# Optimization experiments

Measured on AMD Instinct MI355X. Metric: run time of the kernel, lower is better.

## Reference

```python
import jax, jax.numpy as jnp
import numpy as np

N_U, N_I, D, RANK, NNZ = 100000, 50000, 64, 64, 1000000
L, TEMP, LAMBDA_1, DROPOUT, BATCH_USER, EPS = 2, 0.2, 0.2, 0.1, 2048, 0.05
B = 2048


def _leaky(x):
    return jnp.where(x >= 0, x, 0.5 * x)


def _l2norm(x):
    n = jnp.sqrt(jnp.sum(x * x, axis=1, keepdims=True))
    return x / jnp.maximum(n, 1e-12)


def setup_inputs() -> dict:
    key = jax.random.key(0)
    ks = jax.random.split(key, 24)
    xav = 0.05
    inp = {
        'E_u_0': jax.random.normal(ks[0], (N_U, D), jnp.float32) * xav,
        'E_i_0': jax.random.normal(ks[1], (N_I, D), jnp.float32) * xav,
        'svd_u': jax.random.normal(ks[2], (N_U, RANK), jnp.float32) * xav,
        'svd_v': jax.random.normal(ks[3], (N_I, RANK), jnp.float32) * xav,
        's': jax.random.uniform(ks[4], (RANK,), jnp.float32),
        'ut': jax.random.normal(ks[5], (RANK, N_U), jnp.float32) * xav,
        'vt': jax.random.normal(ks[6], (RANK, N_I), jnp.float32) * xav,
        'W_u': jax.random.normal(ks[7], (L, D, D), jnp.float32) * xav,
        'W_i': jax.random.normal(ks[8], (L, D, D), jnp.float32) * xav,
        'adj_vals': jax.random.uniform(ks[9], (NNZ,), jnp.float32),
        'drop_rand': jax.random.uniform(ks[10], (L, 2, NNZ), jnp.float32),
        'noise_u1': jax.random.uniform(ks[11], (N_U, RANK), jnp.float32),
        'noise_v1': jax.random.uniform(ks[12], (N_I, RANK), jnp.float32),
        'noise_u2': jax.random.uniform(ks[13], (N_U, RANK), jnp.float32),
        'noise_v2': jax.random.uniform(ks[14], (N_I, RANK), jnp.float32),
        'u_mask_raw': jax.random.uniform(ks[15], (L, B), jnp.float32),
        'i_mask_raw': jax.random.uniform(ks[16], (L, B), jnp.float32),
        'adj_rows': jax.random.randint(ks[17], (NNZ,), 0, N_U, jnp.int32),
        'adj_cols': jax.random.randint(ks[18], (NNZ,), 0, N_I, jnp.int32),
        'uids': jax.random.randint(ks[19], (B,), 0, N_U, jnp.int32),
        'iids': jax.random.randint(ks[20], (B,), 0, N_I, jnp.int32),
        'pos': jax.random.randint(ks[21], (B,), 0, N_I, jnp.int32),
        'neg': jax.random.randint(ks[22], (B,), 0, N_I, jnp.int32),
    }
    return inp


def _forward(E_u_0, E_i_0, svd_u, svd_v, s, ut, vt, W_u, W_i, adj_vals,
             drop_rand, noise_u1, noise_v1, noise_u2, noise_v2,
             u_mask_raw, i_mask_raw, adj_rows, adj_cols, uids, iids, pos, neg):
    # --- SVD low-rank augmentation with sign-aligned uniform noise ---
    def perturb(svd, noise):
        return svd + jnp.sign(svd) * _l2norm(noise) * EPS

    svd_u_1, svd_v_1 = perturb(svd_u, noise_u1), perturb(svd_v, noise_v1)
    svd_u_2, svd_v_2 = perturb(svd_u, noise_u2), perturb(svd_v, noise_v2)
    u_mul_s_1 = svd_u_1 * s  # [n_u, r] @ diag(s)
    v_mul_s_1 = svd_v_1 * s
    u_mul_s_2 = svd_u_2 * s
    v_mul_s_2 = svd_v_2 * s

    def spmm_drop(vals_mask_rand, E, seg_ids, gather_ids, n_out):
        keep = (vals_mask_rand >= DROPOUT).astype(adj_vals.dtype)
        dv = adj_vals * keep / (1.0 - DROPOUT)  # sparse dropout w/ rescale
        msgs = dv[:, None] * E[gather_ids]       # [nnz, d]
        return jax.ops.segment_sum(msgs, seg_ids, num_segments=n_out)

    E_u_list, E_i_list = [E_u_0], [E_i_0]
    G_u_1, G_i_1, G_u_2, G_i_2 = [None], [None], [None], [None]
    for layer in range(1, L + 1):
        Eu_p, Ei_p = E_u_list[layer - 1], E_i_list[layer - 1]
        Z_u = _leaky(spmm_drop(drop_rand[layer - 1, 0], Ei_p, adj_rows, adj_cols, N_U))
        Z_i = _leaky(spmm_drop(drop_rand[layer - 1, 1], Eu_p, adj_cols, adj_rows, N_I))
        vt_ei = vt @ Ei_p   # [r, d]
        ut_eu = ut @ Eu_p   # [r, d]
        G_u_1.append(_leaky(u_mul_s_1 @ vt_ei))
        G_i_1.append(_leaky(v_mul_s_1 @ ut_eu))
        G_u_2.append(_leaky(u_mul_s_2 @ vt_ei))
        G_i_2.append(_leaky(v_mul_s_2 @ ut_eu))
        E_u_list.append(Z_u + Eu_p)
        E_i_list.append(Z_i + Ei_p)

    E_u = sum(E_u_list)
    E_i = sum(E_i_list)

    # --- contrastive InfoNCE between the two augmented views ---
    def cl_loss(g1, g2, ids, W, mask_raw):
        mask = (mask_raw > 0.5).astype(g1.dtype)
        h1 = _l2norm(g1[ids]) @ W
        h2 = _l2norm(g2[ids]) @ W
        pos_score = jnp.exp(jnp.sum(h1 * h2, axis=1) / TEMP)
        neg_score = jnp.sum(jnp.exp(h1 @ h2.T / TEMP), axis=1)
        return jnp.sum(-jnp.log(pos_score / (neg_score + 1e-8) + 1e-8) * mask)

    loss_s = jnp.asarray(0.0, E_u.dtype)
    for lyr in range(1, L + 1):
        loss_s = loss_s + cl_loss(G_u_1[lyr], G_u_2[lyr], uids, W_u[lyr - 1], u_mask_raw[lyr - 1])
        loss_s = loss_s + cl_loss(G_i_1[lyr], G_i_2[lyr], iids, W_i[lyr - 1], i_mask_raw[lyr - 1])

    # --- BPR-style hinge loss (vectorized over the batch loop) ---
    u_emb = E_u[uids]
    pos_sc = jnp.sum(u_emb * E_i[pos], axis=1)
    neg_sc = jnp.sum(u_emb * E_i[neg], axis=1)
    loss_r = jnp.sum(jax.nn.relu(1.0 - pos_sc + neg_sc)) / BATCH_USER

    loss = loss_r + LAMBDA_1 * loss_s
    return (loss, loss_r, loss_s)


def reference(E_u_0, E_i_0, svd_u, svd_v, s, ut, vt, W_u, W_i, adj_vals,
              drop_rand, noise_u1, noise_v1, noise_u2, noise_v2,
              u_mask_raw, i_mask_raw, adj_rows, adj_cols, uids, iids, pos, neg):
    return _forward(E_u_0, E_i_0, svd_u, svd_v, s, ut, vt, W_u, W_i, adj_vals,
                    drop_rand, noise_u1, noise_v1, noise_u2, noise_v2,
                    u_mask_raw, i_mask_raw, adj_rows, adj_cols, uids, iids, pos, neg)
```

## Files before the change

kernel.cpp:

```cpp
#include <hip/hip_runtime.h>
#include <cstddef>

#define N_U   100000
#define N_I   50000
#define DD    64
#define NNZ_  1000000
#define LL    2
#define TEMP_ 0.2f
#define LAM1  0.2f
#define DROP_ 0.1f
#define EPS_  0.05f
#define BB    2048
#define KCH   320
#define NCH_I ((N_I + KCH - 1) / KCH)
#define NCH_U ((N_U + KCH - 1) / KCH)
#define REGION_SZ 2097152

#define NBK   391
#define SH_U  8
#define SH_I  7
#define C1_CHUNK   3072
#define C1_THREADS 512
#define C1_EPT     6
#define BH_BLOCKS  256

__device__ __forceinline__ float leaky(float x) { return x >= 0.0f ? x : 0.5f * x; }

__device__ __forceinline__ float waveReduceSum(float v) {
#pragma unroll
  for (int m = 32; m >= 1; m >>= 1) v += __shfl_xor(v, m, 64);
  return v;
}

__device__ __forceinline__ int rlanei(int v, int l) {
  return __builtin_amdgcn_readlane(v, l);
}
__device__ __forceinline__ float rlanef(float v, int l) {
  return __int_as_float(__builtin_amdgcn_readlane(__float_as_int(v), l));
}

__device__ __forceinline__ void gload_lds16(const float* g, float* l) {
  __builtin_amdgcn_global_load_lds(
      (const __attribute__((address_space(1))) void*)g,
      (__attribute__((address_space(3))) void*)l, 16, 0, 0);
}

__global__ void bhist(const int* __restrict__ rows, const int* __restrict__ cols,
                      int* __restrict__ bh) {
  __shared__ int lh[2 * NBK];
  int t = threadIdx.x;
  for (int j = t; j < 2 * NBK; j += 256) lh[j] = 0;
  __syncthreads();
  for (int e = blockIdx.x * 256 + t; e < NNZ_; e += BH_BLOCKS * 256) {
    atomicAdd(&lh[rows[e] >> SH_U], 1);
    atomicAdd(&lh[NBK + (cols[e] >> SH_I)], 1);
  }
  __syncthreads();
  for (int j = t; j < 2 * NBK; j += 256) bh[blockIdx.x * (2 * NBK) + j] = lh[j];
}

__global__ void bscan(const int* __restrict__ bh,
                      int* __restrict__ bbase_u, int* __restrict__ bbase_i,
                      int* __restrict__ bcur_u, int* __restrict__ bcur_i) {
  __shared__ int tot[2 * NBK];
  __shared__ int sc[512];
  int t = threadIdx.x;
  for (int j = t; j < 2 * NBK; j += 256) {
    int s = 0;
    for (int k = 0; k < BH_BLOCKS; ++k) s += bh[k * (2 * NBK) + j];
    tot[j] = s;
  }
  __syncthreads();
  sc[t] = (t < NBK) ? tot[t] : 0;
  sc[t + 256] = (t + 256 < NBK) ? tot[t + 256] : 0;
  __syncthreads();
  for (int ofs = 1; ofs < 512; ofs <<= 1) {
    int a = (t >= ofs) ? sc[t - ofs] : 0;
    int b = (t + 256 >= ofs) ? sc[t + 256 - ofs] : 0;
    __syncthreads();
    sc[t] += a; sc[t + 256] += b;
    __syncthreads();
  }
  if (t == 0) bbase_u[0] = 0;
  for (int j = t; j < NBK; j += 256) bbase_u[j + 1] = sc[j];
  __syncthreads();
  sc[t] = (t < NBK) ? tot[NBK + t] : 0;
  sc[t + 256] = (t + 256 < NBK) ? tot[NBK + t + 256] : 0;
  __syncthreads();
  for (int ofs = 1; ofs < 512; ofs <<= 1) {
    int a = (t >= ofs) ? sc[t - ofs] : 0;
    int b = (t + 256 >= ofs) ? sc[t + 256 - ofs] : 0;
    __syncthreads();
    sc[t] += a; sc[t + 256] += b;
    __syncthreads();
  }
  if (t == 0) bbase_i[0] = 0;
  for (int j = t; j < NBK; j += 256) bbase_i[j + 1] = sc[j];
  for (int j = t; j < NBK; j += 256) { bcur_u[j] = 0; bcur_i[j] = 0; }
}

__global__ __launch_bounds__(C1_THREADS)
void csr_bin(const int* __restrict__ rws, const int* __restrict__ oth,
             const float* __restrict__ vals,
             const float* __restrict__ dA, const float* __restrict__ dB,
             const int* __restrict__ bbase,
             int* __restrict__ bcur,
             float4* __restrict__ stg, int shift) {
  __shared__ float4 st[C1_CHUNK];
  __shared__ int hist[NBK], lbase[NBK], cur2[NBK], slab[NBK], lboff[NBK];
  __shared__ int sc[512];
  int t = threadIdx.x;
  int e0 = blockIdx.x * C1_CHUNK;
  int n = min(C1_CHUNK, NNZ_ - e0);
  for (int b = t; b < NBK; b += C1_THREADS) { hist[b] = 0; cur2[b] = 0; }
  __syncthreads();
  int myr[C1_EPT], myo[C1_EPT];
  float mk1[C1_EPT], mk2[C1_EPT];
#pragma unroll
  for (int k = 0; k < C1_EPT; ++k) {
    int li = t + k * C1_THREADS;
    if (li < n) {
      int e = e0 + li;
      int r = rws[e];
      myr[k] = r;
      myo[k] = oth[e];
      float v = vals[e] * (1.0f / (1.0f - DROP_));
      mk1[k] = (dA[e] >= DROP_) ? v : 0.0f;
      mk2[k] = (dB[e] >= DROP_) ? v : 0.0f;
      atomicAdd(&hist[r >> shift], 1);
    } else {
      myr[k] = -1;
    }
  }
  __syncthreads();
  sc[t] = (t < NBK) ? hist[t] : 0;
  __syncthreads();
  for (int ofs = 1; ofs < 512; ofs <<= 1) {
    int x = (t >= ofs) ? sc[t - ofs] : 0;
    __syncthreads();
    sc[t] += x;
    __syncthreads();
  }
  if (t < NBK) {
    lbase[t] = (t == 0) ? 0 : sc[t - 1];
    lboff[t] = bbase[t];
    if (hist[t] > 0) slab[t] = atomicAdd(&bcur[t], hist[t]);
  }
  __syncthreads();
#pragma unroll
  for (int k = 0; k < C1_EPT; ++k) {
    if (myr[k] >= 0) {
      int b = myr[k] >> shift;
      int pos = lbase[b] + atomicAdd(&cur2[b], 1);
      st[pos] = make_float4(__int_as_float(myo[k]), mk1[k], mk2[k],
                            __int_as_float(myr[k]));
    }
  }
  __syncthreads();
  for (int s = t; s < n; s += C1_THREADS) {
    float4 rec = st[s];
    int r = __float_as_int(rec.w);
    int b = r >> shift;
    stg[(size_t)lboff[b] + slab[b] + (s - lbase[b])] = rec;
  }
}

__global__ void csr_final(const float4* __restrict__ stg, const int* __restrict__ bbase,
                          float2* __restrict__ pay1, float2* __restrict__ pay2,
                          int* __restrict__ off, int N, int shift) {
  __shared__ int h[256], incl[256], cur[256];
  int b = blockIdx.x;
  int t = threadIdx.x;
  int r0 = b << shift;
  int nrows = min(1 << shift, N - r0);
  int lo = bbase[b], hi = bbase[b + 1];
  h[t] = 0; cur[t] = 0;
  __syncthreads();
  for (int i = lo + t; i < hi; i += 256)
    atomicAdd(&h[__float_as_int(stg[i].w) - r0], 1);
  __syncthreads();
  incl[t] = h[t];
  __syncthreads();
  for (int ofs = 1; ofs < 256; ofs <<= 1) {
    int a = (t >= ofs) ? incl[t - ofs] : 0;
    __syncthreads();
    incl[t] += a;
    __syncthreads();
  }
  if (b == 0 && t == 0) off[0] = 0;
  if (t < nrows) off[r0 + t + 1] = lo + incl[t];
  for (int i = lo + t; i < hi; i += 256) {
    float4 rec = stg[i];
    int L = __float_as_int(rec.w) - r0;
    int pos = lo + (incl[L] - h[L]) + atomicAdd(&cur[L], 1);
    pay1[pos] = make_float2(rec.x, rec.y);
    pay2[pos] = make_float2(rec.x, rec.z);
  }
}

__global__ void spmm_all(const int* __restrict__ off_u, const float2* __restrict__ pu,
                         const int* __restrict__ off_i, const float2* __restrict__ pi,
                         const float* __restrict__ Eu0, const float* __restrict__ Ei0,
                         float* __restrict__ EU1, float* __restrict__ EI1) {
  int wid = threadIdx.x >> 6, lane = threadIdx.x & 63;
  int r = blockIdx.x * 4 + wid;
  const int* off; const float2* pay;
  const float* Esrc; const float* base; float* out;
  if (r < N_U) {
    off = off_u; pay = pu; Esrc = Ei0; base = Eu0; out = EU1;
  } else {
    r -= N_U;
    if (r >= N_I) return;
    off = off_i; pay = pi; Esrc = Eu0; base = Ei0; out = EI1;
  }
  int i0 = off[r], i1 = off[r + 1];
  float acc = 0.0f;
  for (int p = i0; p < i1; p += 64) {
    int cn = min(64, i1 - p);
    float dvl = 0.0f; int gl = 0;
    if (lane < cn) {
      float2 pl = pay[p + lane];
      gl = __float_as_int(pl.x);
      dvl = pl.y;
    }
    int j = 0;
    for (; j + 7 < cn; j += 8) {
      float d[8]; int g[8]; float e[8];
#pragma unroll
      for (int q = 0; q < 8; ++q) { d[q] = rlanef(dvl, j + q); g[q] = rlanei(gl, j + q); }
#pragma unroll
      for (int q = 0; q < 8; ++q) e[q] = Esrc[(size_t)g[q] * DD + lane];
#pragma unroll
      for (int q = 0; q < 8; ++q) acc += d[q] * e[q];
    }
    for (; j + 3 < cn; j += 4) {
      float d[4]; int g[4]; float e[4];
#pragma unroll
      for (int q = 0; q < 4; ++q) { d[q] = rlanef(dvl, j + q); g[q] = rlanei(gl, j + q); }
#pragma unroll
      for (int q = 0; q < 4; ++q) e[q] = Esrc[(size_t)g[q] * DD + lane];
#pragma unroll
      for (int q = 0; q < 4; ++q) acc += d[q] * e[q];
    }
    for (; j < cn; ++j)
      acc += rlanef(dvl, j) * Esrc[(size_t)rlanei(gl, j) * DD + lane];
  }
  size_t o = (size_t)r * DD + lane;
  out[o] = base[o] + leaky(acc);
}

__global__ void spmm_batch3(const int* __restrict__ uids, const int* __restrict__ pos,
                            const int* __restrict__ neg,
                            const int* __restrict__ off_u, const float2* __restrict__ pu2,
                            const int* __restrict__ off_i, const float2* __restrict__ pi2,
                            const float* __restrict__ EU1, const float* __restrict__ EI1,
                            float* __restrict__ bu, float* __restrict__ bpos,
                            float* __restrict__ bneg) {
  int z = blockIdx.y;
  const int* ids = (z == 0) ? uids : ((z == 1) ? pos : neg);
  const int* off = (z == 0) ? off_u : off_i;
  const float2* pay = (z == 0) ? pu2 : pi2;
  const float* Esrc = (z == 0) ? EI1 : EU1;
  const float* base = (z == 0) ? EU1 : EI1;
  float* out = (z == 0) ? bu : ((z == 1) ? bpos : bneg);
  int wid = threadIdx.x >> 6, lane = threadIdx.x & 63;
  int i = blockIdx.x * 4 + wid;
  int r = ids[i];
  int i0 = off[r], i1 = off[r + 1];
  float acc = 0.0f;
  for (int p = i0; p < i1; p += 64) {
    int cn = min(64, i1 - p);
    float dvl = 0.0f; int gl = 0;
    if (lane < cn) {
      float2 pl = pay[p + lane];
      gl = __float_as_int(pl.x);
      dvl = pl.y;
    }
    int j = 0;
    for (; j + 7 < cn; j += 8) {
      float d[8]; int g[8]; float e[8];
#pragma unroll
      for (int q = 0; q < 8; ++q) { d[q] = rlanef(dvl, j + q); g[q] = rlanei(gl, j + q); }
#pragma unroll
      for (int q = 0; q < 8; ++q) e[q] = Esrc[(size_t)g[q] * DD + lane];
#pragma unroll
      for (int q = 0; q < 8; ++q) acc += d[q] * e[q];
    }
    for (; j + 3 < cn; j += 4) {
      float d[4]; int g[4]; float e[4];
#pragma unroll
      for (int q = 0; q < 4; ++q) { d[q] = rlanef(dvl, j + q); g[q] = rlanei(gl, j + q); }
#pragma unroll
      for (int q = 0; q < 4; ++q) e[q] = Esrc[(size_t)g[q] * DD + lane];
#pragma unroll
      for (int q = 0; q < 4; ++q) acc += d[q] * e[q];
    }
    for (; j < cn; ++j)
      acc += rlanef(dvl, j) * Esrc[(size_t)rlanei(gl, j) * DD + lane];
  }
  out[(size_t)i * DD + lane] = base[(size_t)r * DD + lane] + leaky(acc);
}

__global__ void gemm_tiled(const float* __restrict__ A0, const float* __restrict__ B0,
                           const float* __restrict__ A1, const float* __restrict__ B1,
                           float* __restrict__ Cp) {
  __shared__ __align__(16) float sA[2][4096];
  __shared__ __align__(16) float sB[2][4096];
  int bx = blockIdx.x;
  const float* A; const float* B; int N; int k0;
  if (bx < NCH_I) { A = A0; B = B0; N = N_I; k0 = bx * KCH; }
  else            { A = A1; B = B1; N = N_U; k0 = (bx - NCH_I) * KCH; }
  int t = threadIdx.x;
  int w = t >> 6, l = t & 63;
  int rseg = l >> 4;
  int c4 = (l & 15) * 4;
  int ti = t >> 4, tj = t & 15;
  int ti4 = ti * 4, tj4 = tj * 4;

  int NT = min(KCH / 64, (N - k0 + 63) >> 6);

  float acc[4][4];
#pragma unroll
  for (int x = 0; x < 4; ++x)
#pragma unroll
    for (int y = 0; y < 4; ++y) acc[x][y] = 0.0f;

  auto stage = [&](int tt, int b) {
    int kb = k0 + tt * 64;
    if (kb + 64 <= N) {
#pragma unroll
      for (int q = 0; q < 4; ++q) {
        int s = w * 4 + q;
        const float* ga = A + (size_t)(s * 4 + rseg) * N + kb + c4;
        gload_lds16(ga, &sA[b][s * 256]);
        const float* gb = B + (size_t)(kb + s * 4 + rseg) * DD + c4;
        gload_lds16(gb, &sB[b][s * 256]);
      }
    } else {
#pragma unroll
      for (int q = 0; q < 16; ++q) {
        int lin = t + q * 256;
        int r = lin >> 6, c = lin & 63;
        sA[b][lin] = (kb + c < N) ? A[(size_t)r * N + kb + c] : 0.0f;
        sB[b][lin] = (kb + r < N) ? B[(size_t)(kb + r) * DD + c] : 0.0f;
      }
    }
  };

  stage(0, 0);
  __syncthreads();
  int cur = 0;
  for (int tt = 0; tt < NT; ++tt) {
    if (tt + 1 < NT) stage(tt + 1, cur ^ 1);
    const float* cA = sA[cur];
    const float* cB = sB[cur];
#pragma unroll 8
    for (int k = 0; k < 64; ++k) {
      float4 b4 = *(const float4*)&cB[k * 64 + tj4];
      float a0 = cA[(ti4 + 0) * 64 + k];
      float a1 = cA[(ti4 + 1) * 64 + k];
      float a2 = cA[(ti4 + 2) * 64 + k];
      float a3 = cA[(ti4 + 3) * 64 + k];
      acc[0][0] += a0 * b4.x; acc[0][1] += a0 * b4.y; acc[0][2] += a0 * b4.z; acc[0][3] += a0 * b4.w;
      acc[1][0] += a1 * b4.x; acc[1][1] += a1 * b4.y; acc[1][2] += a1 * b4.z; acc[1][3] += a1 * b4.w;
      acc[2][0] += a2 * b4.x; acc[2][1] += a2 * b4.y; acc[2][2] += a2 * b4.z; acc[2][3] += a2 * b4.w;
      acc[3][0] += a3 * b4.x; acc[3][1] += a3 * b4.y; acc[3][2] += a3 * b4.z; acc[3][3] += a3 * b4.w;
    }
    __syncthreads();
    cur ^= 1;
  }

  float* cp = Cp + (size_t)bx * 4096;
#pragma unroll
  for (int x = 0; x < 4; ++x)
#pragma unroll
    for (int y = 0; y < 4; ++y)
      cp[(ti4 + x) * DD + tj4 + y] = acc[x][y];
}

__global__ void gemm_reduce_s1(const float* __restrict__ Cp, float* __restrict__ Cp2) {
  int y = blockIdx.y, z = blockIdx.z;
  const float* base = Cp + (y ? (size_t)NCH_I * 4096 : 0);
  int cnt = y ? NCH_U : NCH_I;
  int chunk = (cnt + 3) >> 2;
  int b0 = z * chunk, b1 = min(b0 + chunk, cnt);
  int idx = blockIdx.x * 256 + threadIdx.x;
  float s = 0.0f;
  for (int b = b0; b < b1; ++b) s += base[(size_t)b * 4096 + idx];
  Cp2[((size_t)(y * 4 + z)) * 4096 + idx] = s;
}

__global__ void gemm_reduce_s2(const float* __restrict__ Cp2,
                               float* __restrict__ C0, float* __restrict__ C1) {
  int y = blockIdx.y;
  float* C = y ? C1 : C0;
  int idx = blockIdx.x * 256 + threadIdx.x;
  float s = 0.0f;
#pragma unroll
  for (int z = 0; z < 4; ++z) s += Cp2[((size_t)(y * 4 + z)) * 4096 + idx];
  C[idx] = s;
}

__global__ void h_kernel2(const float* __restrict__ svd,
                          const float* __restrict__ n1, const float* __restrict__ n2,
                          const float* __restrict__ sdiag,
                          const float* __restrict__ Mb,
                          const float* __restrict__ Wb,
                          const int*   __restrict__ ids,
                          float*       __restrict__ hout) {
  int layer = blockIdx.y;
  const float* M = Mb + layer * 4096;
  const float* W = Wb + layer * 4096;
  int wid  = threadIdx.x >> 6;
  int lane = threadIdx.x & 63;
  int i = blockIdx.x * 4 + wid;
  int id = ids[i];
  float sv = svd[(size_t)id * DD + lane];
  float sgn = (sv > 0.0f) ? 1.0f : ((sv < 0.0f) ? -1.0f : 0.0f);
  float sd = sdiag[lane];

  float z1 = n1[(size_t)id * DD + lane];
  float z2 = n2[(size_t)id * DD + lane];
  float d1 = fmaxf(sqrtf(waveReduceSum(z1 * z1)), 1e-12f);
  float d2 = fmaxf(sqrtf(waveReduceSum(z2 * z2)), 1e-12f);
  float g1 = (sv + sgn * (z1 / d1) * EPS_) * sd;
  float g2 = (sv + sgn * (z2 / d2) * EPS_) * sd;

  float a1 = 0.0f, a2 = 0.0f;
#pragma unroll
  for (int k = 0; k < 64; ++k) {
    float m = M[k * DD + lane];
    a1 += rlanef(g1, k) * m;
    a2 += rlanef(g2, k) * m;
  }
  a1 = leaky(a1); a2 = leaky(a2);
  float s1 = fmaxf(sqrtf(waveReduceSum(a1 * a1)), 1e-12f);
  float s2 = fmaxf(sqrtf(waveReduceSum(a2 * a2)), 1e-12f);
  float gn1 = a1 / s1, gn2 = a2 / s2;

  float h1 = 0.0f, h2 = 0.0f;
#pragma unroll
  for (int k = 0; k < 64; ++k) {
    float w = W[k * DD + lane];
    h1 += rlanef(gn1, k) * w;
    h2 += rlanef(gn2, k) * w;
  }
  size_t b0 = ((size_t)(layer * 2 + 0) * BB + i) * DD + lane;
  size_t b1 = ((size_t)(layer * 2 + 1) * BB + i) * DD + lane;
  hout[b0] = h1;
  hout[b1] = h2;
}

__global__ void score_tiles(const float* __restrict__ hu, const float* __restrict__ hv,
                            float* __restrict__ negpart) {
  __shared__ float s1[64][65];
  __shared__ float s2[64][65];
  int z = blockIdx.z;
  int layer = z >> 1, side = z & 1;
  const float* hb = side ? hv : hu;
  const float* h1 = hb + (size_t)(layer * 2 + 0) * BB * DD;
  const float* h2 = hb + (size_t)(layer * 2 + 1) * BB * DD;
  int i0 = blockIdx.x * 64, j0 = blockIdx.y * 64;
  int t = threadIdx.x;
#pragma unroll
  for (int k = 0; k < 16; ++k) {
    int lin = t + k * 256;
    int r = lin >> 6, c = lin & 63;
    s1[r][c] = h1[(size_t)(i0 + r) * DD + c];
    s2[r][c] = h2[(size_t)(j0 + r) * DD + c];
  }
  __syncthreads();
  int ti = t >> 4, tj = t & 15;
  float acc[4][4];
#pragma unroll
  for (int x = 0; x < 4; ++x)
#pragma unroll
    for (int y = 0; y < 4; ++y) acc[x][y] = 0.0f;
  for (int d = 0; d < 64; ++d) {
    float a[4], b[4];
#pragma unroll
    for (int k = 0; k < 4; ++k) { a[k] = s1[ti * 4 + k][d]; b[k] = s2[tj * 4 + k][d]; }
#pragma unroll
    for (int x = 0; x < 4; ++x)
#pragma unroll
      for (int y = 0; y < 4; ++y) acc[x][y] += a[x] * b[y];
  }
  float rsum[4];
#pragma unroll
  for (int x = 0; x < 4; ++x) {
    float s = 0.0f;
#pragma unroll
    for (int y = 0; y < 4; ++y) s += expf(acc[x][y] * (1.0f / TEMP_));
    rsum[x] = s;
  }
  __syncthreads();
#pragma unroll
  for (int x = 0; x < 4; ++x) s1[ti * 4 + x][tj] = rsum[x];
  __syncthreads();
  if (t < 64) {
    float s = 0.0f;
#pragma unroll
    for (int c = 0; c < 16; ++c) s += s1[t][c];
    negpart[((size_t)z * 32 + blockIdx.y) * BB + i0 + t] = s;
  }
}

__global__ void score_loss(const float* __restrict__ hu, const float* __restrict__ hv,
                           const float* __restrict__ negpart,
                           const float* __restrict__ u_mask, const float* __restrict__ i_mask,
                           float* __restrict__ loss_acc) {
  __shared__ float red[256];
  int z = blockIdx.y;
  int layer = z >> 1, side = z & 1;
  const float* hb = side ? hv : hu;
  const float* h1 = hb + (size_t)(layer * 2 + 0) * BB * DD;
  const float* h2 = hb + (size_t)(layer * 2 + 1) * BB * DD;
  const float* mask = (side ? i_mask : u_mask) + layer * BB;
  int i = blockIdx.x * 256 + threadIdx.x;
  const float4* a = (const float4*)(h1 + (size_t)i * DD);
  const float4* b = (const float4*)(h2 + (size_t)i * DD);
  float pos = 0.0f;
#pragma unroll
  for (int k = 0; k < 16; ++k) {
    float4 av = a[k], bv = b[k];
    pos += av.x * bv.x + av.y * bv.y + av.z * bv.z + av.w * bv.w;
  }
  float ng = 0.0f;
  for (int jt = 0; jt < 32; ++jt) ng += negpart[((size_t)z * 32 + jt) * BB + i];
  float ps = expf(pos * (1.0f / TEMP_));
  float m = (mask[i] > 0.5f) ? 1.0f : 0.0f;
  float li = -logf(ps / (ng + 1e-8f) + 1e-8f) * m;
  red[threadIdx.x] = li;
  __syncthreads();
  for (int ofs = 128; ofs >= 1; ofs >>= 1) {
    if (threadIdx.x < ofs) red[threadIdx.x] += red[threadIdx.x + ofs];
    __syncthreads();
  }
  if (threadIdx.x == 0) unsafeAtomicAdd(loss_acc, red[0]);
}

__global__ void bpr_kernel(const float* __restrict__ Eu0, const float* __restrict__ EU1,
                           const float* __restrict__ bu,
                           const float* __restrict__ Ei0, const float* __restrict__ EI1,
                           const float* __restrict__ bpos, const float* __restrict__ bneg,
                           const int* __restrict__ uids, const int* __restrict__ pos,
                           const int* __restrict__ neg,
                           float* __restrict__ acc_r) {
  __shared__ float red[256];
  int i = blockIdx.x * 256 + threadIdx.x;
  const float4* u0 = (const float4*)(Eu0 + (size_t)uids[i] * DD);
  const float4* u1 = (const float4*)(EU1 + (size_t)uids[i] * DD);
  const float4* u2 = (const float4*)(bu  + (size_t)i * DD);
  const float4* p0 = (const float4*)(Ei0 + (size_t)pos[i] * DD);
  const float4* p1 = (const float4*)(EI1 + (size_t)pos[i] * DD);
  const float4* p2 = (const float4*)(bpos + (size_t)i * DD);
  const float4* n0 = (const float4*)(Ei0 + (size_t)neg[i] * DD);
  const float4* n1 = (const float4*)(EI1 + (size_t)neg[i] * DD);
  const float4* n2 = (const float4*)(bneg + (size_t)i * DD);
  float ps = 0.0f, ns = 0.0f;
#pragma unroll
  for (int k = 0; k < 16; ++k) {
    float4 ua = u0[k], ub = u1[k], uc = u2[k];
    float4 pa = p0[k], pb = p1[k], pc = p2[k];
    float4 na = n0[k], nb = n1[k], nc = n2[k];
    float ux = ua.x + ub.x + uc.x, uy = ua.y + ub.y + uc.y,
          uz = ua.z + ub.z + uc.z, uw = ua.w + ub.w + uc.w;
    ps += ux * (pa.x + pb.x + pc.x) + uy * (pa.y + pb.y + pc.y)
        + uz * (pa.z + pb.z + pc.z) + uw * (pa.w + pb.w + pc.w);
    ns += ux * (na.x + nb.x + nc.x) + uy * (na.y + nb.y + nc.y)
        + uz * (na.z + nb.z + nc.z) + uw * (na.w + nb.w + nc.w);
  }
  red[threadIdx.x] = fmaxf(1.0f - ps + ns, 0.0f);
  __syncthreads();
  for (int ofs = 128; ofs >= 1; ofs >>= 1) {
    if (threadIdx.x < ofs) red[threadIdx.x] += red[threadIdx.x + ofs];
    __syncthreads();
  }
  if (threadIdx.x == 0) unsafeAtomicAdd(acc_r, red[0]);
}

__global__ void finalize_kernel(const float* __restrict__ acc, float* __restrict__ out) {
  float lr = acc[0] / (float)BB;
  float ls = acc[1];
  out[0] = lr + LAM1 * ls;
  out[1] = lr;
  out[2] = ls;
}

extern "C" void kernel_launch(void* const* d_in, const int* in_sizes, int n_in,
                              void* d_out, int out_size, void* d_ws, size_t ws_size,
                              hipStream_t stream) {
  const float* E_u_0   = (const float*)d_in[0];
  const float* E_i_0   = (const float*)d_in[1];
  const float* svd_u   = (const float*)d_in[2];
  const float* svd_v   = (const float*)d_in[3];
  const float* sdiag   = (const float*)d_in[4];
  const float* ut      = (const float*)d_in[5];
  const float* vt      = (const float*)d_in[6];
  const float* W_u     = (const float*)d_in[7];
  const float* W_i     = (const float*)d_in[8];
  const float* adjv    = (const float*)d_in[9];
  const float* dropr   = (const float*)d_in[10];
  const float* noise_u1= (const float*)d_in[11];
  const float* noise_v1= (const float*)d_in[12];
  const float* noise_u2= (const float*)d_in[13];
  const float* noise_v2= (const float*)d_in[14];
  const float* u_mask  = (const float*)d_in[15];
  const float* i_mask  = (const float*)d_in[16];
  const int*   rows    = (const int*)d_in[17];
  const int*   cols    = (const int*)d_in[18];
  const int*   uids    = (const int*)d_in[19];
  const int*   iids    = (const int*)d_in[20];
  const int*   pos     = (const int*)d_in[21];
  const int*   neg     = (const int*)d_in[22];
  float* out = (float*)d_out;

  float* ws     = (float*)d_ws;
  float* EU1    = ws;
  float* EI1    = EU1 + (size_t)N_U * DD;
  float* vtei   = EI1 + (size_t)N_I * DD;
  float* uteu   = vtei + 2 * DD * DD;
  float* accs   = uteu + 2 * DD * DD;
  float* region = accs + 16;
  float* Cp   = region;
  float* Cp2  = Cp + (size_t)(NCH_I + NCH_U) * 4096;
  float* bu   = region;
  float* bpos = bu   + (size_t)BB * DD;
  float* bneg = bpos + (size_t)BB * DD;
  float* hu   = bneg + (size_t)BB * DD;
  float* hv   = hu   + (size_t)4 * BB * DD;
  float* negp = hv   + (size_t)4 * BB * DD;
  float2* pay1_u = (float2*)(region + (size_t)REGION_SZ);
  float2* pay2_u = pay1_u + NNZ_;
  float2* pay1_i = pay2_u + NNZ_;
  float2* pay2_i = pay1_i + NNZ_;
  int* off_u   = (int*)(pay2_i + NNZ_);
  int* off_i   = off_u + (N_U + 1);
  int* bcur_u  = off_i + (N_I + 1);
  int* bcur_i  = bcur_u + NBK;
  int* bbase_u = bcur_i + NBK;
  int* bbase_i = bbase_u + (NBK + 1);
  float4* stg_u = (float4*)ws;
  float4* stg_i = stg_u + NNZ_;
  int* bh = (int*)region;

  const int TB = 256;
  dim3 blk(TB);
  int row_grid = BB / 4;

  hipMemsetAsync(accs, 0, 16 * sizeof(float), stream);

  bhist<<<BH_BLOCKS, blk, 0, stream>>>(rows, cols, bh);
  bscan<<<1, blk, 0, stream>>>(bh, bbase_u, bbase_i, bcur_u, bcur_i);
  {
    int c1g = (NNZ_ + C1_CHUNK - 1) / C1_CHUNK;
    csr_bin<<<c1g, C1_THREADS, 0, stream>>>(rows, cols, adjv,
        dropr, dropr + (size_t)2 * NNZ_, bbase_u, bcur_u, stg_u, SH_U);
    csr_bin<<<c1g, C1_THREADS, 0, stream>>>(cols, rows, adjv,
        dropr + (size_t)NNZ_, dropr + (size_t)3 * NNZ_, bbase_i, bcur_i, stg_i, SH_I);
    csr_final<<<NBK, blk, 0, stream>>>(stg_u, bbase_u, pay1_u, pay2_u, off_u, N_U, SH_U);
    csr_final<<<NBK, blk, 0, stream>>>(stg_i, bbase_i, pay1_i, pay2_i, off_i, N_I, SH_I);
  }

  gemm_tiled<<<NCH_I + NCH_U, blk, 0, stream>>>(vt, E_i_0, ut, E_u_0, Cp);
  gemm_reduce_s1<<<dim3(16, 2, 4), blk, 0, stream>>>(Cp, Cp2);
  gemm_reduce_s2<<<dim3(16, 2), blk, 0, stream>>>(Cp2, vtei, uteu);

  spmm_all<<<(N_U + N_I + 3) / 4, blk, 0, stream>>>(off_u, pay1_u, off_i, pay1_i,
                                                    E_u_0, E_i_0, EU1, EI1);

  gemm_tiled<<<NCH_I + NCH_U, blk, 0, stream>>>(vt, EI1, ut, EU1, Cp);
  gemm_reduce_s1<<<dim3(16, 2, 4), blk, 0, stream>>>(Cp, Cp2);
  gemm_reduce_s2<<<dim3(16, 2), blk, 0, stream>>>(Cp2, vtei + 4096, uteu + 4096);

  spmm_batch3<<<dim3(row_grid, 3), blk, 0, stream>>>(uids, pos, neg,
      off_u, pay2_u, off_i, pay2_i, EU1, EI1, bu, bpos, bneg);

  h_kernel2<<<dim3(row_grid, LL), blk, 0, stream>>>(svd_u, noise_u1, noise_u2, sdiag,
                                                    vtei, W_u, uids, hu);
  h_kernel2<<<dim3(row_grid, LL), blk, 0, stream>>>(svd_v, noise_v1, noise_v2, sdiag,
                                                    uteu, W_i, iids, hv);
  score_tiles<<<dim3(32, 32, 4), blk, 0, stream>>>(hu, hv, negp);
  score_loss<<<dim3(8, 4), blk, 0, stream>>>(hu, hv, negp, u_mask, i_mask, accs + 1);

  bpr_kernel<<<8, blk, 0, stream>>>(E_u_0, EU1, bu, E_i_0, EI1, bpos, bneg,
                                    uids, pos, neg, accs);

  finalize_kernel<<<1, 1, 0, stream>>>(accs, out);
}
```

Measured before the change: 624.7 us.

## Merge paired launches, vectorize SpMM gathers, parallelize BPR per wavefront

The user-side and item-side launches of csr_bin, csr_final and h_kernel2 are merged into single launches that pick the side from a grid dimension, which cuts launch overhead and lets both sides run at once. The SpMM gather now has each group of 16 lanes load a float4 slice of an embedding row, so one wavefront fetches four neighbours per step, and it sums the groups with xor shuffles. The BPR kernel moves from one thread per sample with serial float4 loops to one wavefront per sample with a wave reduction, giving more parallelism on a small batch. The new gather loop steps by 8 without tail handling and relies on lanes past the count carrying zero weights, which adds wasted loads on short rows.

```diff
diff --git a/kernel.cpp b/kernel.cpp
--- a/kernel.cpp
+++ b/kernel.cpp
@@ -100,12 +100,21 @@
 }
 
 __global__ __launch_bounds__(C1_THREADS)
-void csr_bin(const int* __restrict__ rws, const int* __restrict__ oth,
-             const float* __restrict__ vals,
-             const float* __restrict__ dA, const float* __restrict__ dB,
-             const int* __restrict__ bbase,
-             int* __restrict__ bcur,
-             float4* __restrict__ stg, int shift) {
+void csr_bin(const int* __restrict__ rows, const int* __restrict__ cols,
+             const float* __restrict__ vals, const float* __restrict__ dropr,
+             const int* __restrict__ bbase_u, const int* __restrict__ bbase_i,
+             int* __restrict__ bcur_u, int* __restrict__ bcur_i,
+             float4* __restrict__ stg_u, float4* __restrict__ stg_i) {
+  int side = blockIdx.y;
+  const int* rws = side ? cols : rows;
+  const int* oth = side ? rows : cols;
+  const float* dA = dropr + (side ? (size_t)NNZ_ : 0);
+  const float* dB = dropr + (side ? (size_t)3 * NNZ_ : (size_t)2 * NNZ_);
+  const int* bbase = side ? bbase_i : bbase_u;
+  int* bcur = side ? bcur_i : bcur_u;
+  float4* stg = side ? stg_i : stg_u;
+  int shift = side ? SH_I : SH_U;
+
   __shared__ float4 st[C1_CHUNK];
   __shared__ int hist[NBK], lbase[NBK], cur2[NBK], slab[NBK], lboff[NBK];
   __shared__ int sc[512];
@@ -165,9 +174,20 @@
   }
 }
 
-__global__ void csr_final(const float4* __restrict__ stg, const int* __restrict__ bbase,
-                          float2* __restrict__ pay1, float2* __restrict__ pay2,
-                          int* __restrict__ off, int N, int shift) {
+__global__ void csr_final(const float4* __restrict__ stg_u, const float4* __restrict__ stg_i,
+                          const int* __restrict__ bbase_u, const int* __restrict__ bbase_i,
+                          float2* __restrict__ pay1_u, float2* __restrict__ pay2_u,
+                          float2* __restrict__ pay1_i, float2* __restrict__ pay2_i,
+                          int* __restrict__ off_u, int* __restrict__ off_i) {
+  int side = blockIdx.y;
+  const float4* stg = side ? stg_i : stg_u;
+  const int* bbase = side ? bbase_i : bbase_u;
+  float2* pay1 = side ? pay1_i : pay1_u;
+  float2* pay2 = side ? pay2_i : pay2_u;
+  int* off = side ? off_i : off_u;
+  int N = side ? N_I : N_U;
+  int shift = side ? SH_I : SH_U;
+
   __shared__ int h[256], incl[256], cur[256];
   int b = blockIdx.x;
   int t = threadIdx.x;
@@ -198,23 +218,12 @@
   }
 }
 
-__global__ void spmm_all(const int* __restrict__ off_u, const float2* __restrict__ pu,
-                         const int* __restrict__ off_i, const float2* __restrict__ pi,
-                         const float* __restrict__ Eu0, const float* __restrict__ Ei0,
-                         float* __restrict__ EU1, float* __restrict__ EI1) {
-  int wid = threadIdx.x >> 6, lane = threadIdx.x & 63;
-  int r = blockIdx.x * 4 + wid;
-  const int* off; const float2* pay;
-  const float* Esrc; const float* base; float* out;
-  if (r < N_U) {
-    off = off_u; pay = pu; Esrc = Ei0; base = Eu0; out = EU1;
-  } else {
-    r -= N_U;
-    if (r >= N_I) return;
-    off = off_i; pay = pi; Esrc = Eu0; base = Ei0; out = EI1;
-  }
+__device__ __forceinline__ float4 spmm_gather(const int* __restrict__ off,
+                                              const float2* __restrict__ pay,
+                                              const float* __restrict__ Esrc,
+                                              int r, int lane, int g, int s) {
   int i0 = off[r], i1 = off[r + 1];
-  float acc = 0.0f;
+  float4 acc = make_float4(0.f, 0.f, 0.f, 0.f);
   for (int p = i0; p < i1; p += 64) {
     int cn = min(64, i1 - p);
     float dvl = 0.0f; int gl = 0;
@@ -223,30 +232,51 @@
       gl = __float_as_int(pl.x);
       dvl = pl.y;
     }
-    int j = 0;
-    for (; j + 7 < cn; j += 8) {
-      float d[8]; int g[8]; float e[8];
-#pragma unroll
-      for (int q = 0; q < 8; ++q) { d[q] = rlanef(dvl, j + q); g[q] = rlanei(gl, j + q); }
-#pragma unroll
-      for (int q = 0; q < 8; ++q) e[q] = Esrc[(size_t)g[q] * DD + lane];
-#pragma unroll
-      for (int q = 0; q < 8; ++q) acc += d[q] * e[q];
+    for (int j = 0; j < cn; j += 8) {
+      int ga = __shfl(gl, j + g, 64);
+      float da = __shfl(dvl, j + g, 64);
+      int gb = __shfl(gl, j + 4 + g, 64);
+      float db = __shfl(dvl, j + 4 + g, 64);
+      float4 ea = *((const float4*)(Esrc + (size_t)ga * DD) + s);
+      float4 eb = *((const float4*)(Esrc + (size_t)gb * DD) + s);
+      acc.x += da * ea.x; acc.y += da * ea.y; acc.z += da * ea.z; acc.w += da * ea.w;
+      acc.x += db * eb.x; acc.y += db * eb.y; acc.z += db * eb.z; acc.w += db * eb.w;
     }
-    for (; j + 3 < cn; j += 4) {
-      float d[4]; int g[4]; float e[4];
-#pragma unroll
-      for (int q = 0; q < 4; ++q) { d[q] = rlanef(dvl, j + q); g[q] = rlanei(gl, j + q); }
-#pragma unroll
-      for (int q = 0; q < 4; ++q) e[q] = Esrc[(size_t)g[q] * DD + lane];
-#pragma unroll
-      for (int q = 0; q < 4; ++q) acc += d[q] * e[q];
-    }
-    for (; j < cn; ++j)
-      acc += rlanef(dvl, j) * Esrc[(size_t)rlanei(gl, j) * DD + lane];
-  }
-  size_t o = (size_t)r * DD + lane;
-  out[o] = base[o] + leaky(acc);
+  }
+#pragma unroll
+  for (int m = 16; m <= 32; m <<= 1) {
+    acc.x += __shfl_xor(acc.x, m, 64);
+    acc.y += __shfl_xor(acc.y, m, 64);
+    acc.z += __shfl_xor(acc.z, m, 64);
+    acc.w += __shfl_xor(acc.w, m, 64);
+  }
+  return acc;
+}
+
+__global__ void spmm_all(const int* __restrict__ off_u, const float2* __restrict__ pu,
+                         const int* __restrict__ off_i, const float2* __restrict__ pi,
+                         const float* __restrict__ Eu0, const float* __restrict__ Ei0,
+                         float* __restrict__ EU1, float* __restrict__ EI1) {
+  int wid = threadIdx.x >> 6, lane = threadIdx.x & 63;
+  int g = lane >> 4, s = lane & 15;
+  int r = blockIdx.x * 4 + wid;
+  const int* off; const float2* pay;
+  const float* Esrc; const float* base; float* outp;
+  if (r < N_U) {
+    off = off_u; pay = pu; Esrc = Ei0; base = Eu0; outp = EU1;
+  } else {
+    r -= N_U;
+    if (r >= N_I) return;
+    off = off_i; pay = pi; Esrc = Eu0; base = Ei0; outp = EI1;
+  }
+  float4 acc = spmm_gather(off, pay, Esrc, r, lane, g, s);
+  if (g == 0) {
+    float4 bb = *((const float4*)(base + (size_t)r * DD) + s);
+    float4 o;
+    o.x = bb.x + leaky(acc.x); o.y = bb.y + leaky(acc.y);
+    o.z = bb.z + leaky(acc.z); o.w = bb.w + leaky(acc.w);
+    *((float4*)(outp + (size_t)r * DD) + s) = o;
+  }
 }
 
 __global__ void spmm_batch3(const int* __restrict__ uids, const int* __restrict__ pos,
@@ -262,43 +292,19 @@
   const float2* pay = (z == 0) ? pu2 : pi2;
   const float* Esrc = (z == 0) ? EI1 : EU1;
   const float* base = (z == 0) ? EU1 : EI1;
-  float* out = (z == 0) ? bu : ((z == 1) ? bpos : bneg);
+  float* outp = (z == 0) ? bu : ((z == 1) ? bpos : bneg);
   int wid = threadIdx.x >> 6, lane = threadIdx.x & 63;
+  int g = lane >> 4, s = lane & 15;
   int i = blockIdx.x * 4 + wid;
   int r = ids[i];
-  int i0 = off[r], i1 = off[r + 1];
-  float acc = 0.0f;
-  for (int p = i0; p < i1; p += 64) {
-    int cn = min(64, i1 - p);
-    float dvl = 0.0f; int gl = 0;
-    if (lane < cn) {
-      float2 pl = pay[p + lane];
-      gl = __float_as_int(pl.x);
-      dvl = pl.y;
-    }
-    int j = 0;
-    for (; j + 7 < cn; j += 8) {
-      float d[8]; int g[8]; float e[8];
-#pragma unroll
-      for (int q = 0; q < 8; ++q) { d[q] = rlanef(dvl, j + q); g[q] = rlanei(gl, j + q); }
-#pragma unroll
-      for (int q = 0; q < 8; ++q) e[q] = Esrc[(size_t)g[q] * DD + lane];
-#pragma unroll
-      for (int q = 0; q < 8; ++q) acc += d[q] * e[q];
-    }
-    for (; j + 3 < cn; j += 4) {
-      float d[4]; int g[4]; float e[4];
-#pragma unroll
-      for (int q = 0; q < 4; ++q) { d[q] = rlanef(dvl, j + q); g[q] = rlanei(gl, j + q); }
-#pragma unroll
-      for (int q = 0; q < 4; ++q) e[q] = Esrc[(size_t)g[q] * DD + lane];
-#pragma unroll
-      for (int q = 0; q < 4; ++q) acc += d[q] * e[q];
-    }
-    for (; j < cn; ++j)
-      acc += rlanef(dvl, j) * Esrc[(size_t)rlanei(gl, j) * DD + lane];
-  }
-  out[(size_t)i * DD + lane] = base[(size_t)r * DD + lane] + leaky(acc);
+  float4 acc = spmm_gather(off, pay, Esrc, r, lane, g, s);
+  if (g == 0) {
+    float4 bb = *((const float4*)(base + (size_t)r * DD) + s);
+    float4 o;
+    o.x = bb.x + leaky(acc.x); o.y = bb.y + leaky(acc.y);
+    o.z = bb.z + leaky(acc.z); o.w = bb.w + leaky(acc.w);
+    *((float4*)(outp + (size_t)i * DD) + s) = o;
+  }
 }
 
 __global__ void gemm_tiled(const float* __restrict__ A0, const float* __restrict__ B0,
@@ -401,13 +407,23 @@
   C[idx] = s;
 }
 
-__global__ void h_kernel2(const float* __restrict__ svd,
-                          const float* __restrict__ n1, const float* __restrict__ n2,
+__global__ void h_kernel2(const float* __restrict__ svd_u, const float* __restrict__ svd_v,
+                          const float* __restrict__ n1u, const float* __restrict__ n2u,
+                          const float* __restrict__ n1v, const float* __restrict__ n2v,
                           const float* __restrict__ sdiag,
-                          const float* __restrict__ Mb,
-                          const float* __restrict__ Wb,
-                          const int*   __restrict__ ids,
-                          float*       __restrict__ hout) {
+                          const float* __restrict__ Mu, const float* __restrict__ Mv,
+                          const float* __restrict__ Wu, const float* __restrict__ Wv,
+                          const int* __restrict__ uids, const int* __restrict__ iids,
+                          float* __restrict__ hu, float* __restrict__ hv) {
+  int side = blockIdx.z;
+  const float* svd = side ? svd_v : svd_u;
+  const float* n1 = side ? n1v : n1u;
+  const float* n2 = side ? n2v : n2u;
+  const float* Mb = side ? Mv : Mu;
+  const float* Wb = side ? Wv : Wu;
+  const int* ids = side ? iids : uids;
+  float* hout = side ? hv : hu;
+
   int layer = blockIdx.y;
   const float* M = Mb + layer * 4096;
   const float* W = Wb + layer * 4096;
@@ -546,37 +562,22 @@
                            const int* __restrict__ uids, const int* __restrict__ pos,
                            const int* __restrict__ neg,
                            float* __restrict__ acc_r) {
-  __shared__ float red[256];
-  int i = blockIdx.x * 256 + threadIdx.x;
-  const float4* u0 = (const float4*)(Eu0 + (size_t)uids[i] * DD);
-  const float4* u1 = (const float4*)(EU1 + (size_t)uids[i] * DD);
-  const float4* u2 = (const float4*)(bu  + (size_t)i * DD);
-  const float4* p0 = (const float4*)(Ei0 + (size_t)pos[i] * DD);
-  const float4* p1 = (const float4*)(EI1 + (size_t)pos[i] * DD);
-  const float4* p2 = (const float4*)(bpos + (size_t)i * DD);
-  const float4* n0 = (const float4*)(Ei0 + (size_t)neg[i] * DD);
-  const float4* n1 = (const float4*)(EI1 + (size_t)neg[i] * DD);
-  const float4* n2 = (const float4*)(bneg + (size_t)i * DD);
-  float ps = 0.0f, ns = 0.0f;
-#pragma unroll
-  for (int k = 0; k < 16; ++k) {
-    float4 ua = u0[k], ub = u1[k], uc = u2[k];
-    float4 pa = p0[k], pb = p1[k], pc = p2[k];
-    float4 na = n0[k], nb = n1[k], nc = n2[k];
-    float ux = ua.x + ub.x + uc.x, uy = ua.y + ub.y + uc.y,
-          uz = ua.z + ub.z + uc.z, uw = ua.w + ub.w + uc.w;
-    ps += ux * (pa.x + pb.x + pc.x) + uy * (pa.y + pb.y + pc.y)
-        + uz * (pa.z + pb.z + pc.z) + uw * (pa.w + pb.w + pc.w);
-    ns += ux * (na.x + nb.x + nc.x) + uy * (na.y + nb.y + nc.y)
-        + uz * (na.z + nb.z + nc.z) + uw * (na.w + nb.w + nc.w);
-  }
-  red[threadIdx.x] = fmaxf(1.0f - ps + ns, 0.0f);
-  __syncthreads();
-  for (int ofs = 128; ofs >= 1; ofs >>= 1) {
-    if (threadIdx.x < ofs) red[threadIdx.x] += red[threadIdx.x + ofs];
-    __syncthreads();
-  }
-  if (threadIdx.x == 0) unsafeAtomicAdd(acc_r, red[0]);
+  __shared__ float red[4];
+  int wid = threadIdx.x >> 6, lane = threadIdx.x & 63;
+  int i = blockIdx.x * 4 + wid;
+  int u = uids[i], p = pos[i], n = neg[i];
+  float ue = Eu0[(size_t)u * DD + lane] + EU1[(size_t)u * DD + lane]
+           + bu[(size_t)i * DD + lane];
+  float pe = Ei0[(size_t)p * DD + lane] + EI1[(size_t)p * DD + lane]
+           + bpos[(size_t)i * DD + lane];
+  float ne = Ei0[(size_t)n * DD + lane] + EI1[(size_t)n * DD + lane]
+           + bneg[(size_t)i * DD + lane];
+  float ps = waveReduceSum(ue * pe);
+  float ns = waveReduceSum(ue * ne);
+  if (lane == 0) red[wid] = fmaxf(1.0f - ps + ns, 0.0f);
+  __syncthreads();
+  if (threadIdx.x == 0)
+    unsafeAtomicAdd(acc_r, red[0] + red[1] + red[2] + red[3]);
 }
 
 __global__ void finalize_kernel(const float* __restrict__ acc, float* __restrict__ out) {
@@ -654,12 +655,10 @@
   bscan<<<1, blk, 0, stream>>>(bh, bbase_u, bbase_i, bcur_u, bcur_i);
   {
     int c1g = (NNZ_ + C1_CHUNK - 1) / C1_CHUNK;
-    csr_bin<<<c1g, C1_THREADS, 0, stream>>>(rows, cols, adjv,
-        dropr, dropr + (size_t)2 * NNZ_, bbase_u, bcur_u, stg_u, SH_U);
-    csr_bin<<<c1g, C1_THREADS, 0, stream>>>(cols, rows, adjv,
-        dropr + (size_t)NNZ_, dropr + (size_t)3 * NNZ_, bbase_i, bcur_i, stg_i, SH_I);
-    csr_final<<<NBK, blk, 0, stream>>>(stg_u, bbase_u, pay1_u, pay2_u, off_u, N_U, SH_U);
-    csr_final<<<NBK, blk, 0, stream>>>(stg_i, bbase_i, pay1_i, pay2_i, off_i, N_I, SH_I);
+    csr_bin<<<dim3(c1g, 2), C1_THREADS, 0, stream>>>(rows, cols, adjv, dropr,
+        bbase_u, bbase_i, bcur_u, bcur_i, stg_u, stg_i);
+    csr_final<<<dim3(NBK, 2), blk, 0, stream>>>(stg_u, stg_i, bbase_u, bbase_i,
+        pay1_u, pay2_u, pay1_i, pay2_i, off_u, off_i);
   }
 
   gemm_tiled<<<NCH_I + NCH_U, blk, 0, stream>>>(vt, E_i_0, ut, E_u_0, Cp);
@@ -676,15 +675,14 @@
   spmm_batch3<<<dim3(row_grid, 3), blk, 0, stream>>>(uids, pos, neg,
       off_u, pay2_u, off_i, pay2_i, EU1, EI1, bu, bpos, bneg);
 
-  h_kernel2<<<dim3(row_grid, LL), blk, 0, stream>>>(svd_u, noise_u1, noise_u2, sdiag,
-                                                    vtei, W_u, uids, hu);
-  h_kernel2<<<dim3(row_grid, LL), blk, 0, stream>>>(svd_v, noise_v1, noise_v2, sdiag,
-                                                    uteu, W_i, iids, hv);
+  h_kernel2<<<dim3(row_grid, LL, 2), blk, 0, stream>>>(svd_u, svd_v,
+      noise_u1, noise_u2, noise_v1, noise_v2, sdiag,
+      vtei, uteu, W_u, W_i, uids, iids, hu, hv);
   score_tiles<<<dim3(32, 32, 4), blk, 0, stream>>>(hu, hv, negp);
   score_loss<<<dim3(8, 4), blk, 0, stream>>>(hu, hv, negp, u_mask, i_mask, accs + 1);
 
-  bpr_kernel<<<8, blk, 0, stream>>>(E_u_0, EU1, bu, E_i_0, EI1, bpos, bneg,
-                                    uids, pos, neg, accs);
+  bpr_kernel<<<row_grid, blk, 0, stream>>>(E_u_0, EU1, bu, E_i_0, EI1, bpos, bneg,
+                                           uids, pos, neg, accs);
 
   finalize_kernel<<<1, 1, 0, stream>>>(accs, out);
 }
```

New measurement: 589.1 us. 5.7% less time.
